# Performance work log

Measured on AMD Instinct MI355X. Metric: run time of the kernel, lower is better.

The kernel has to match this reference:

```python
import jax, jax.numpy as jnp
import numpy as np

NUM_HEADS = 16


def setup_inputs() -> dict:
    key = jax.random.key(0)
    ks = jax.random.split(key, 6)
    B, S, D = 2, 2048, 1024
    hidden_states = jax.random.normal(ks[0], (B, S, D), dtype=jnp.float32)
    attention_mask = jnp.zeros((B, 1, 1, S), dtype=jnp.float32)  # additive mask
    # Linear weights stored as [in, out] (equivalent to torch weight.T)
    W_qkv = jax.random.normal(ks[1], (D, 3 * D), dtype=jnp.float32) * (1.0 / np.sqrt(D))
    b_qkv = jnp.zeros((3 * D,), dtype=jnp.float32)
    W_proj = jax.random.normal(ks[2], (D, D), dtype=jnp.float32) * (1.0 / np.sqrt(D))
    b_proj = jnp.zeros((D,), dtype=jnp.float32)
    return {
        "hidden_states": hidden_states,
        "attention_mask": attention_mask,
        "W_qkv": W_qkv,
        "b_qkv": b_qkv,
        "W_proj": W_proj,
        "b_proj": b_proj,
    }


def reference(hidden_states, attention_mask, W_qkv, b_qkv, W_proj, b_proj):
    B, S, D = hidden_states.shape
    H = NUM_HEADS
    hd = D // H
    scale = 1.0 / jnp.sqrt(jnp.asarray(hd, hidden_states.dtype))

    qkv = hidden_states @ W_qkv + b_qkv            # [B,S,3D]
    q, k, v = jnp.split(qkv, 3, axis=-1)
    # [B,S,D] -> [B,H,S,hd]
    split_heads = lambda t: t.reshape(B, S, H, hd).transpose(0, 2, 1, 3)
    q, k, v = split_heads(q), split_heads(k), split_heads(v)

    scores = jnp.einsum("bhqd,bhkd->bhqk", q, k) * scale + attention_mask
    attn = jax.nn.softmax(scores, axis=-1)
    ctx = jnp.einsum("bhqk,bhkd->bhqd", attn, v)   # [B,H,S,hd]
    ctx = ctx.transpose(0, 2, 1, 3).reshape(B, S, D)
    return ctx @ W_proj + b_proj
```

## Files before the change

### kernel.cpp

```cpp
#include <hip/hip_runtime.h>
#include <hip/hip_bf16.h>

typedef short short8 __attribute__((ext_vector_type(8)));
typedef float floatx4 __attribute__((ext_vector_type(4)));

#define S_LEN 2048
#define DMODEL 1024
#define NH 16
#define HD 64
#define BATCH 2

static __device__ __forceinline__ short f2bf(float x) {
    __hip_bfloat16 h = __float2bfloat16(x);
    return *(short*)&h;
}

static __device__ __forceinline__ void async_ld16(const __hip_bfloat16* g, __hip_bfloat16* l) {
    __builtin_amdgcn_global_load_lds(
        (const __attribute__((address_space(1))) unsigned int*)g,
        (__attribute__((address_space(3))) unsigned int*)l, 16, 0, 0);
}

__global__ __launch_bounds__(256) void cvt_kernel(const float* __restrict__ X,
                                                  __hip_bfloat16* __restrict__ Y) {
    int i = (blockIdx.x * 256 + threadIdx.x) * 8;
    floatx4 f0 = *(const floatx4*)&X[i];
    floatx4 f1 = *(const floatx4*)&X[i + 4];
    short8 s;
    s[0] = f2bf(f0[0]); s[1] = f2bf(f0[1]); s[2] = f2bf(f0[2]); s[3] = f2bf(f0[3]);
    s[4] = f2bf(f1[0]); s[5] = f2bf(f1[1]); s[6] = f2bf(f1[2]); s[7] = f2bf(f1[3]);
    *(short8*)&Y[i] = s;
}

__global__ void transpose_kernel(const float* __restrict__ W,
                                 __hip_bfloat16* __restrict__ Wt, int K, int N) {
    __shared__ float tile[32][33];
    int n0 = blockIdx.x * 32, k0 = blockIdx.y * 32;
    int tx = threadIdx.x, ty = threadIdx.y;
#pragma unroll
    for (int i = 0; i < 32; i += 8)
        tile[ty + i][tx] = W[(size_t)(k0 + ty + i) * N + n0 + tx];
    __syncthreads();
#pragma unroll
    for (int i = 0; i < 32; i += 8)
        Wt[(size_t)(n0 + ty + i) * K + k0 + tx] = __float2bfloat16(tile[tx][ty + i]);
}

__global__ __launch_bounds__(256) void gemm128(
    const __hip_bfloat16* __restrict__ A, const __hip_bfloat16* __restrict__ Bt,
    const float* __restrict__ bias, float* __restrict__ Cf,
    __hip_bfloat16* __restrict__ Qp, __hip_bfloat16* __restrict__ Kp,
    __hip_bfloat16* __restrict__ Vt, int M, int N, int K, int mode) {
    __shared__ __align__(16) __hip_bfloat16 As[128 * 32];
    __shared__ __align__(16) __hip_bfloat16 Bs[128 * 32];
    const int m0 = blockIdx.y * 128, n0 = blockIdx.x * 128;
    const int t = threadIdx.x;
    const int wave = t >> 6, lane = t & 63;
    const int quad = lane >> 4, m16 = lane & 15;
    const int wm = (wave >> 1) * 64, wn = (wave & 1) * 64;
    const int srow = lane >> 2, scol = (lane & 3) * 8;

    floatx4 acc[4][4] = {};
    for (int k0 = 0; k0 < K; k0 += 32) {
#pragma unroll
        for (int i = 0; i < 2; i++) {
            const int rbase = wave * 32 + i * 16;
            async_ld16(&A[(size_t)(m0 + rbase + srow) * K + k0 + scol], &As[rbase * 32]);
            async_ld16(&Bt[(size_t)(n0 + rbase + srow) * K + k0 + scol], &Bs[rbase * 32]);
        }
        __syncthreads();
        short8 af[4], bfr[4];
#pragma unroll
        for (int i = 0; i < 4; i++)
            af[i] = *(const short8*)&As[(wm + i * 16 + m16) * 32 + quad * 8];
#pragma unroll
        for (int j = 0; j < 4; j++)
            bfr[j] = *(const short8*)&Bs[(wn + j * 16 + m16) * 32 + quad * 8];
#pragma unroll
        for (int i = 0; i < 4; i++)
#pragma unroll
            for (int j = 0; j < 4; j++)
                acc[i][j] = __builtin_amdgcn_mfma_f32_16x16x32_bf16(af[i], bfr[j], acc[i][j], 0, 0, 0);
        __syncthreads();
    }
#pragma unroll
    for (int i = 0; i < 4; i++)
#pragma unroll
        for (int j = 0; j < 4; j++) {
            int col = n0 + wn + j * 16 + m16;
            float bv = bias[col];
#pragma unroll
            for (int r = 0; r < 4; r++) {
                int row = m0 + wm + i * 16 + quad * 4 + r;
                float v = acc[i][j][r] + bv;
                if (mode == 0) {
                    Cf[(size_t)row * N + col] = v;
                } else {
                    __hip_bfloat16 hv = __float2bfloat16(v);
                    int tt = col >> 10, rem = col & 1023;
                    int h = rem >> 6, d = rem & 63;
                    int b = row >> 11, s = row & 2047;
                    if (tt == 0)      Qp[((size_t)(b * NH + h) * S_LEN + s) * HD + d] = hv;
                    else if (tt == 1) Kp[((size_t)(b * NH + h) * S_LEN + s) * HD + d] = hv;
                    else              Vt[((size_t)(b * NH + h) * HD + d) * S_LEN + s] = hv;
                }
            }
        }
}

__global__ __launch_bounds__(256) void attn_kernel(
    const __hip_bfloat16* __restrict__ Q,
    const __hip_bfloat16* __restrict__ K,
    const __hip_bfloat16* __restrict__ Vt,
    const float* __restrict__ mask,
    __hip_bfloat16* __restrict__ ctx) {
    __shared__ __align__(16) __hip_bfloat16 Ks[2][32 * 64];
    __shared__ __align__(16) __hip_bfloat16 Vs[2][64 * 32];
    __shared__ __align__(16) __hip_bfloat16 Ps[4][16][40];
    const int bh = blockIdx.x;
    const int b = bh >> 4, h = bh & 15;
    const int t = threadIdx.x, wave = t >> 6, lane = t & 63;
    const int quad = lane >> 4, m16 = lane & 15;
    const int qbase = blockIdx.y * 64 + wave * 16;
    const __hip_bfloat16* Qh = Q + (size_t)bh * S_LEN * HD;
    const __hip_bfloat16* Kh = K + (size_t)bh * S_LEN * HD;
    const __hip_bfloat16* Vh = Vt + (size_t)bh * HD * S_LEN;
    const float* mb = mask + (size_t)b * S_LEN;
    const float scale = 0.125f;
    const float M_FIX = 20.0f;

    const int kr = lane >> 3, kc = lane & 7;
    const size_t kgoff = (size_t)(wave * 8 + kr) * HD + ((kc ^ (kr & 7)) * 8);
    const int vr = lane >> 2, vc = lane & 3;
    const size_t vgoff = (size_t)(wave * 16 + vr) * S_LEN + ((vc ^ (vr & 3)) * 8);
    __hip_bfloat16* kdst0 = &Ks[0][wave * 512]; __hip_bfloat16* kdst1 = &Ks[1][wave * 512];
    __hip_bfloat16* vdst0 = &Vs[0][wave * 512]; __hip_bfloat16* vdst1 = &Vs[1][wave * 512];

    short8 aq0 = *(const short8*)&Qh[(size_t)(qbase + m16) * HD + quad * 8];
    short8 aq1 = *(const short8*)&Qh[(size_t)(qbase + m16) * HD + 32 + quad * 8];

    async_ld16(&Kh[kgoff], kdst0);
    async_ld16(&Vh[vgoff], vdst0);
    __syncthreads();

    floatx4 o[4] = {};
    float li[4] = {0.f, 0.f, 0.f, 0.f};

    const int swk = m16 & 7;
    for (int it = 0; it < S_LEN / 32; it++) {
        const int k0 = it * 32;
        const int cur = it & 1;
        if (it < S_LEN / 32 - 1) {
            async_ld16(&Kh[(size_t)(k0 + 32) * HD + kgoff], cur ? kdst0 : kdst1);
            async_ld16(&Vh[(size_t)(k0 + 32) + vgoff], cur ? vdst0 : vdst1);
        }

        const __hip_bfloat16* Kc = Ks[cur];
        short8 bk00 = *(const short8*)&Kc[m16 * 64 + ((quad ^ swk) * 8)];
        short8 bk01 = *(const short8*)&Kc[m16 * 64 + (((quad + 4) ^ swk) * 8)];
        short8 bk10 = *(const short8*)&Kc[(16 + m16) * 64 + ((quad ^ swk) * 8)];
        short8 bk11 = *(const short8*)&Kc[(16 + m16) * 64 + (((quad + 4) ^ swk) * 8)];
        floatx4 sc0 = {}, sc1 = {};
        sc0 = __builtin_amdgcn_mfma_f32_16x16x32_bf16(aq0, bk00, sc0, 0, 0, 0);
        sc0 = __builtin_amdgcn_mfma_f32_16x16x32_bf16(aq1, bk01, sc0, 0, 0, 0);
        sc1 = __builtin_amdgcn_mfma_f32_16x16x32_bf16(aq0, bk10, sc1, 0, 0, 0);
        sc1 = __builtin_amdgcn_mfma_f32_16x16x32_bf16(aq1, bk11, sc1, 0, 0, 0);

        float mk0 = mb[k0 + m16] - M_FIX;
        float mk1 = mb[k0 + 16 + m16] - M_FIX;
#pragma unroll
        for (int r = 0; r < 4; r++) {
            float p0 = __expf(sc0[r] * scale + mk0);
            float p1 = __expf(sc1[r] * scale + mk1);
            li[r] += p0 + p1;
            Ps[wave][quad * 4 + r][m16] = __float2bfloat16(p0);
            Ps[wave][quad * 4 + r][16 + m16] = __float2bfloat16(p1);
        }
        short8 ap = *(const short8*)&Ps[wave][m16][quad * 8];
        const __hip_bfloat16* Vc = Vs[cur];
#pragma unroll
        for (int tt = 0; tt < 4; tt++) {
            const int d = tt * 16 + m16;
            short8 bv = *(const short8*)&Vc[d * 32 + ((quad ^ (d & 3)) * 8)];
            o[tt] = __builtin_amdgcn_mfma_f32_16x16x32_bf16(ap, bv, o[tt], 0, 0, 0);
        }
        __syncthreads();
    }

#pragma unroll
    for (int r = 0; r < 4; r++) {
#pragma unroll
        for (int off = 1; off < 16; off <<= 1)
            li[r] += __shfl_xor(li[r], off, 16);
        li[r] = 1.0f / li[r];
    }
#pragma unroll
    for (int tt = 0; tt < 4; tt++)
#pragma unroll
        for (int r = 0; r < 4; r++) {
            int srow = qbase + quad * 4 + r;
            int d = tt * 16 + m16;
            float v = o[tt][r] * li[r];
            ctx[((size_t)b * S_LEN + srow) * DMODEL + h * HD + d] = __float2bfloat16(v);
        }
}

extern "C" void kernel_launch(void* const* d_in, const int* in_sizes, int n_in,
                              void* d_out, int out_size, void* d_ws, size_t ws_size,
                              hipStream_t stream) {
    (void)in_sizes; (void)n_in; (void)out_size; (void)ws_size;
    const float* hidden = (const float*)d_in[0];
    const float* mask   = (const float*)d_in[1];
    const float* Wqkv   = (const float*)d_in[2];
    const float* bqkv   = (const float*)d_in[3];
    const float* Wproj  = (const float*)d_in[4];
    const float* bproj  = (const float*)d_in[5];
    float* out = (float*)d_out;

    __hip_bfloat16* ws = (__hip_bfloat16*)d_ws;
    const size_t Q4 = 4u * 1024 * 1024;
    __hip_bfloat16* Qp      = ws;
    __hip_bfloat16* Kp      = ws + 1 * Q4;
    __hip_bfloat16* Vt      = ws + 2 * Q4;
    __hip_bfloat16* hid_bf  = ws + 3 * Q4;
    __hip_bfloat16* ctx     = ws + 3 * Q4;
    __hip_bfloat16* Wqkv_t  = ws + 4 * Q4;
    __hip_bfloat16* Wproj_t = ws + 4 * Q4;

    cvt_kernel<<<dim3(4 * 1024 * 1024 / 2048), 256, 0, stream>>>(hidden, hid_bf);
    transpose_kernel<<<dim3(3072 / 32, 1024 / 32), dim3(32, 8), 0, stream>>>(Wqkv, Wqkv_t, 1024, 3072);

    gemm128<<<dim3(3072 / 128, 4096 / 128), 256, 0, stream>>>(
        hid_bf, Wqkv_t, bqkv, nullptr, Qp, Kp, Vt, BATCH * S_LEN, 3 * DMODEL, DMODEL, 1);

    transpose_kernel<<<dim3(1024 / 32, 1024 / 32), dim3(32, 8), 0, stream>>>(Wproj, Wproj_t, 1024, 1024);

    attn_kernel<<<dim3(BATCH * NH, S_LEN / 64), 256, 0, stream>>>(Qp, Kp, Vt, mask, ctx);

    gemm128<<<dim3(1024 / 128, 4096 / 128), 256, 0, stream>>>(
        ctx, Wproj_t, bproj, out, nullptr, nullptr, nullptr, BATCH * S_LEN, DMODEL, DMODEL, 0);
}
```

Measured before the change: 228.1 us.

## Use exp2, MFMA row-sum, swizzled P tile and MFMA priority in attention

Folds log2(e) into the scale and mask so the softmax uses the native exp2 instruction. Computes the row sums with an extra MFMA against a ones vector, which drops the per-element adds and the final shuffle reduction. Swizzles the P staging tile in LDS to reduce bank conflicts, and raises wave priority around the MFMA blocks. Row sums now come from bf16-rounded P, which slightly changes normalization numerics.

```diff
diff --git a/kernel.cpp b/kernel.cpp
--- a/kernel.cpp
+++ b/kernel.cpp
@@ -126,8 +126,9 @@
     const __hip_bfloat16* Kh = K + (size_t)bh * S_LEN * HD;
     const __hip_bfloat16* Vh = Vt + (size_t)bh * HD * S_LEN;
     const float* mb = mask + (size_t)b * S_LEN;
-    const float scale = 0.125f;
-    const float M_FIX = 20.0f;
+    const float LOG2E = 1.44269504f;
+    const float scale2 = 0.125f * LOG2E;
+    const float M_FIX2 = 20.0f * LOG2E;
 
     const int kr = lane >> 3, kc = lane & 7;
     const size_t kgoff = (size_t)(wave * 8 + kr) * HD + ((kc ^ (kr & 7)) * 8);
@@ -139,14 +140,21 @@
     short8 aq0 = *(const short8*)&Qh[(size_t)(qbase + m16) * HD + quad * 8];
     short8 aq1 = *(const short8*)&Qh[(size_t)(qbase + m16) * HD + 32 + quad * 8];
 
+    const short ONEB = (short)0x3F80;
+    const short8 ones = {ONEB, ONEB, ONEB, ONEB, ONEB, ONEB, ONEB, ONEB};
+
     async_ld16(&Kh[kgoff], kdst0);
     async_ld16(&Vh[vgoff], vdst0);
     __syncthreads();
 
     floatx4 o[4] = {};
-    float li[4] = {0.f, 0.f, 0.f, 0.f};
+    floatx4 lacc = {};
 
     const int swk = m16 & 7;
+    const int pc0 = (((m16 >> 3) ^ quad) << 3) | (m16 & 7);
+    const int pc1 = ((((m16 >> 3) + 2) ^ quad) << 3) | (m16 & 7);
+    const int apoff = (quad ^ ((m16 >> 2) & 3)) * 8;
+
     for (int it = 0; it < S_LEN / 32; it++) {
         const int k0 = it * 32;
         const int cur = it & 1;
@@ -161,39 +169,39 @@
         short8 bk10 = *(const short8*)&Kc[(16 + m16) * 64 + ((quad ^ swk) * 8)];
         short8 bk11 = *(const short8*)&Kc[(16 + m16) * 64 + (((quad + 4) ^ swk) * 8)];
         floatx4 sc0 = {}, sc1 = {};
+        __builtin_amdgcn_s_setprio(1);
         sc0 = __builtin_amdgcn_mfma_f32_16x16x32_bf16(aq0, bk00, sc0, 0, 0, 0);
         sc0 = __builtin_amdgcn_mfma_f32_16x16x32_bf16(aq1, bk01, sc0, 0, 0, 0);
         sc1 = __builtin_amdgcn_mfma_f32_16x16x32_bf16(aq0, bk10, sc1, 0, 0, 0);
         sc1 = __builtin_amdgcn_mfma_f32_16x16x32_bf16(aq1, bk11, sc1, 0, 0, 0);
-
-        float mk0 = mb[k0 + m16] - M_FIX;
-        float mk1 = mb[k0 + 16 + m16] - M_FIX;
+        __builtin_amdgcn_s_setprio(0);
+
+        float mk0 = mb[k0 + m16] * LOG2E - M_FIX2;
+        float mk1 = mb[k0 + 16 + m16] * LOG2E - M_FIX2;
 #pragma unroll
         for (int r = 0; r < 4; r++) {
-            float p0 = __expf(sc0[r] * scale + mk0);
-            float p1 = __expf(sc1[r] * scale + mk1);
-            li[r] += p0 + p1;
-            Ps[wave][quad * 4 + r][m16] = __float2bfloat16(p0);
-            Ps[wave][quad * 4 + r][16 + m16] = __float2bfloat16(p1);
-        }
-        short8 ap = *(const short8*)&Ps[wave][m16][quad * 8];
+            float p0 = __builtin_amdgcn_exp2f(sc0[r] * scale2 + mk0);
+            float p1 = __builtin_amdgcn_exp2f(sc1[r] * scale2 + mk1);
+            Ps[wave][quad * 4 + r][pc0] = __float2bfloat16(p0);
+            Ps[wave][quad * 4 + r][pc1] = __float2bfloat16(p1);
+        }
+        short8 ap = *(const short8*)&Ps[wave][m16][apoff];
         const __hip_bfloat16* Vc = Vs[cur];
+        __builtin_amdgcn_s_setprio(1);
+        lacc = __builtin_amdgcn_mfma_f32_16x16x32_bf16(ap, ones, lacc, 0, 0, 0);
 #pragma unroll
         for (int tt = 0; tt < 4; tt++) {
             const int d = tt * 16 + m16;
             short8 bv = *(const short8*)&Vc[d * 32 + ((quad ^ (d & 3)) * 8)];
             o[tt] = __builtin_amdgcn_mfma_f32_16x16x32_bf16(ap, bv, o[tt], 0, 0, 0);
         }
+        __builtin_amdgcn_s_setprio(0);
         __syncthreads();
     }
 
-#pragma unroll
-    for (int r = 0; r < 4; r++) {
-#pragma unroll
-        for (int off = 1; off < 16; off <<= 1)
-            li[r] += __shfl_xor(li[r], off, 16);
-        li[r] = 1.0f / li[r];
-    }
+    float li[4];
+#pragma unroll
+    for (int r = 0; r < 4; r++) li[r] = 1.0f / lacc[r];
 #pragma unroll
     for (int tt = 0; tt < 4; tt++)
 #pragma unroll
```

New measurement: 228.5 us. Within noise of the previous version (+0.2%).
